# Optimization experiments

Hardware: AMD Instinct MI355X
Metric: run time of the kernel (lower is better)

## Reference

```python
import jax, jax.numpy as jnp
import numpy as np

B, S, E, H, WIN = 16, 4096, 512, 8, 64


def setup_inputs() -> dict:
    key = jax.random.key(0)
    k1, k2, k3 = jax.random.split(key, 3)
    bound = 1.0 / np.sqrt(E)
    x = jax.random.normal(k1, (B, S, E), dtype=jnp.float32)
    # nn.MultiheadAttention params: packed in-projection (3E, E) + bias, out-projection (E, E) + bias
    W_in = jax.random.uniform(k2, (3 * E, E), minval=-bound, maxval=bound, dtype=jnp.float32)
    b_in = jnp.zeros((3 * E,), dtype=jnp.float32)
    W_out = jax.random.uniform(k3, (E, E), minval=-bound, maxval=bound, dtype=jnp.float32)
    b_out = jnp.zeros((E,), dtype=jnp.float32)
    return {"x": x, "W_in": W_in, "b_in": b_in, "W_out": W_out, "b_out": b_out}


def reference(x, W_in, b_in, W_out, b_out):
    # Faithful to the torch module: nn.MultiheadAttention has batch_first=False,
    # over the batch axis, with window positions acting as the MHA batch.
    Bb, Ss, Ee = x.shape
    Dh = Ee // H
    nW = Ss // WIN
    xp = x.reshape(Bb, nW, WIN, Ee).transpose(1, 2, 0, 3)
    qkv = xp @ W_in.T + b_in
    q, k, v = jnp.split(qkv, 3, axis=-1)
    q = q.reshape(nW, WIN, Bb, H, Dh)
    k = k.reshape(nW, WIN, Bb, H, Dh)
    v = v.reshape(nW, WIN, Bb, H, Dh)
    scale = 1.0 / np.sqrt(Dh)
    scores = jnp.einsum('nwahd,nwbhd->nwhab', q, k) * scale
    attn = jax.nn.softmax(scores, axis=-1)
    o = jnp.einsum('nwhab,nwbhd->nwahd', attn, v).reshape(nW, WIN, Bb, Ee)
    out = o @ W_out.T + b_out
    return out.transpose(2, 0, 1, 3).reshape(Bb, Ss, Ee)
```

## Files before the change

kernel.cpp:

```cpp
#include <hip/hip_runtime.h>


#define S_LEN  4096
#define E_DIM  512
#define QKV_LD 1536

typedef __bf16 bf16x8 __attribute__((ext_vector_type(8)));
typedef __bf16 bf16x4 __attribute__((ext_vector_type(4)));
typedef short  s16x4  __attribute__((ext_vector_type(4)));
typedef float  f32x4  __attribute__((ext_vector_type(4)));

__device__ __forceinline__ float b2f(unsigned int u16) {
    return __uint_as_float(u16 << 16);
}
__device__ __forceinline__ unsigned short f2bf(float f) {
    unsigned int u = __float_as_uint(f);
    u += 0x7fffu + ((u >> 16) & 1u);
    return (unsigned short)(u >> 16);
}
__device__ __forceinline__ void unpack8(uint4 u, float* f) {
    f[0] = b2f(u.x & 0xffffu); f[1] = b2f(u.x >> 16);
    f[2] = b2f(u.y & 0xffffu); f[3] = b2f(u.y >> 16);
    f[4] = b2f(u.z & 0xffffu); f[5] = b2f(u.z >> 16);
    f[6] = b2f(u.w & 0xffffu); f[7] = b2f(u.w >> 16);
}
__device__ __forceinline__ uint4 pack8(const float* f) {
    uint4 u;
    u.x = (unsigned)f2bf(f[0]) | ((unsigned)f2bf(f[1]) << 16);
    u.y = (unsigned)f2bf(f[2]) | ((unsigned)f2bf(f[3]) << 16);
    u.z = (unsigned)f2bf(f[4]) | ((unsigned)f2bf(f[5]) << 16);
    u.w = (unsigned)f2bf(f[6]) | ((unsigned)f2bf(f[7]) << 16);
    return u;
}

__device__ __forceinline__ bool detect_f32(const unsigned int* __restrict__ probe) {
    unsigned int w = probe[threadIdx.x & 63];
    unsigned int e = (w >> 23) & 0xffu;
    unsigned long long b = __ballot(e >= 90u && e <= 160u);
    return __popcll(b) >= 32;
}

__device__ __forceinline__ void gload16(const unsigned short* g, unsigned short* l) {
    __builtin_amdgcn_global_load_lds(
        (const __attribute__((address_space(1))) unsigned int*)g,
        (__attribute__((address_space(3))) unsigned int*)l, 16, 0, 0);
}

__device__ __forceinline__ f32x4 mfma16bf(s16x4 a, s16x4 b, f32x4 c) {
    f32x4 d;
    asm volatile("s_nop 3\n\t"
                 "v_mfma_f32_16x16x16_bf16 %0, %1, %2, %3\n\t"
                 "s_nop 7\n\t"
                 "s_nop 7"
                 : "=v"(d) : "v"(a), "v"(b), "v"(c));
    return d;
}

template<bool F32>
__device__ __forceinline__ uint4 cvt8(const void* src, long off) {
    if (F32) {
        const float* p = (const float*)src + off;
        float4 a = *(const float4*)p, b = *(const float4*)(p + 4);
        float f[8] = {a.x, a.y, a.z, a.w, b.x, b.y, b.z, b.w};
        return pack8(f);
    }
    return *(const uint4*)((const unsigned short*)src + off);
}

template<bool F32>
__device__ void conv_w_body(const void* Win, const void* Wout, const void* bin,
                            const void* bout, unsigned short* dst)
{
    int c = blockIdx.x * 256 + threadIdx.x;
    if (c >= 131328) return;
    const void* src; long soff; long doff = (long)c * 8;
    if (c < 98304)       { src = Win;  soff = doff; }
    else if (c < 131072) { src = Wout; soff = doff - 786432; }
    else if (c < 131264) { src = bin;  soff = doff - 1048576; }
    else                 { src = bout; soff = doff - 1050112; }
    *(uint4*)(dst + doff) = cvt8<F32>(src, soff);
}
__global__ __launch_bounds__(256) void conv_w_k(const void* Win, const void* Wout,
        const void* bin, const void* bout, unsigned short* dst,
        const unsigned int* __restrict__ probe)
{
    if (detect_f32(probe)) conv_w_body<true>(Win, Wout, bin, bout, dst);
    else                   conv_w_body<false>(Win, Wout, bin, bout, dst);
}

template<bool F32>
__device__ void conv_x_body(const void* __restrict__ x, unsigned short* __restrict__ xb,
                            int s0, int lgC)
{
    long c = (long)blockIdx.x * 256 + threadIdx.x;
    const long row = c >> 6;
    const int  col = (int)(c & 63) * 8;
    const long srcRow = (row >> lgC) * S_LEN + s0 + (row & ((1L << lgC) - 1));
    *(uint4*)(xb + row * E_DIM + col) = cvt8<F32>(x, srcRow * E_DIM + col);
}
__global__ __launch_bounds__(256) void conv_x_k(const void* __restrict__ x,
        unsigned short* __restrict__ xb, int s0, int lgC,
        const unsigned int* __restrict__ probe)
{
    if (detect_f32(probe)) conv_x_body<true>(x, xb, s0, lgC);
    else                   conv_x_body<false>(x, xb, s0, lgC);
}

template<int BM, int BN, int WM, int WN, int MODE>
__device__ void gemm8_body(const unsigned short* __restrict__ A,
                           const unsigned short* __restrict__ W,
                           const unsigned short* __restrict__ bias,
                           void* __restrict__ C, int s0, int lgC, int nbx,
                           bool f32out)
{
    constexpr int MF   = BM / WM / 16;
    constexpr int NF   = BN / WN / 16;
    constexpr int NL   = (BM + BN) / 64;
    constexpr int TILE = (BM + BN) * 64;
    constexpr int NT   = E_DIM / 64;
    constexpr int lda  = (MODE == 1) ? E_DIM : QKV_LD;

    __shared__ __align__(16) unsigned short Ls[2 * TILE];

    const int nwg = gridDim.x;
    const int id0 = blockIdx.x;
    const int id  = (id0 & 7) * (nwg >> 3) + (id0 >> 3);
    const int bx  = id % nbx;
    const int by  = id / nbx;

    const int tid  = threadIdx.x;
    const int wave = tid >> 6;
    const int lane = tid & 63;
    const int wm   = wave / WN;
    const int wn   = wave % WN;
    const int lrow = lane & 15;
    const int lq   = lane >> 4;
    const long m0  = (long)bx * BM;
    const int  n0  = by * BN;

    const unsigned short* src[NL];
    unsigned short*       dst[NL];
    #pragma unroll
    for (int j = 0; j < NL; ++j) {
        const int Lg  = wave * NL + j;
        const int row = Lg * 8 + (lane >> 3);
        const int ls  = (lane & 7) ^ (row & 7);
        src[j] = (row < BM) ? A + (m0 + row) * lda + ls * 8
                            : W + (long)(n0 + row - BM) * E_DIM + ls * 8;
        dst[j] = Ls + Lg * 512;
    }

    f32x4 acc[MF][NF];
    #pragma unroll
    for (int i = 0; i < MF; ++i)
        #pragma unroll
        for (int j = 0; j < NF; ++j)
            acc[i][j] = (f32x4){0.f, 0.f, 0.f, 0.f};

    #pragma unroll
    for (int j = 0; j < NL; ++j) gload16(src[j], dst[j]);

    int buf = 0;
    #pragma unroll
    for (int it = 0; it < NT; ++it) {
        __builtin_amdgcn_s_barrier();
        asm volatile("" ::: "memory");
        if (it + 1 < NT) {
            #pragma unroll
            for (int j = 0; j < NL; ++j)
                gload16(src[j] + (it + 1) * 64, dst[j] + (buf ^ 1) * TILE);
            asm volatile("s_waitcnt vmcnt(%0)" :: "n"(NL) : "memory");
        } else {
            asm volatile("s_waitcnt vmcnt(0)" ::: "memory");
        }
        __builtin_amdgcn_sched_barrier(0);
        __builtin_amdgcn_s_barrier();
        asm volatile("" ::: "memory");

        const unsigned short* Ab = Ls + buf * TILE;
        const unsigned short* Bb = Ab + BM * 64;
        #pragma unroll
        for (int ks = 0; ks < 2; ++ks) {
            bf16x8 bfr[NF];
            #pragma unroll
            for (int ni = 0; ni < NF; ++ni) {
                const int r = wn * (BN / WN) + ni * 16 + lrow;
                bfr[ni] = *(const bf16x8*)(Bb + r * 64 + (((ks * 4 + lq) ^ (r & 7)) << 3));
            }
            #pragma unroll
            for (int mh = 0; mh < MF; mh += 4) {
                bf16x8 afr[4];
                #pragma unroll
                for (int u = 0; u < 4; ++u) {
                    const int r = wm * (BM / WM) + (mh + u) * 16 + lrow;
                    afr[u] = *(const bf16x8*)(Ab + r * 64 + (((ks * 4 + lq) ^ (r & 7)) << 3));
                }
                __builtin_amdgcn_s_setprio(1);
                #pragma unroll
                for (int u = 0; u < 4; ++u)
                    #pragma unroll
                    for (int ni = 0; ni < NF; ++ni)
                        acc[mh + u][ni] = __builtin_amdgcn_mfma_f32_16x16x32_bf16(
                            afr[u], bfr[ni], acc[mh + u][ni], 0, 0, 0);
                __builtin_amdgcn_s_setprio(0);
            }
        }
        __builtin_amdgcn_sched_barrier(0);
        buf ^= 1;
    }

    #pragma unroll
    for (int mi = 0; mi < MF; ++mi)
        #pragma unroll
        for (int ni = 0; ni < NF; ++ni) {
            const int col = n0 + wn * (BN / WN) + ni * 16 + lrow;
            const float bv = b2f(bias[col]);
            #pragma unroll
            for (int r = 0; r < 4; ++r) {
                const long row = m0 + wm * (BM / WM) + mi * 16 + lq * 4 + r;
                const float v = acc[mi][ni][r] + bv;
                if (MODE == 1) {
                    ((unsigned short*)C)[row * QKV_LD + col] = f2bf(v);
                } else {
                    const long g = ((row >> lgC) * S_LEN + s0 + (row & ((1L << lgC) - 1)))
                                   * E_DIM + col;
                    if (f32out) ((float*)C)[g] = v;
                    else        ((unsigned short*)C)[g] = f2bf(v);
                }
            }
        }
}

__global__ __launch_bounds__(512, 2) void gemm1_k(const unsigned short* __restrict__ A,
        const unsigned short* __restrict__ W, const unsigned short* __restrict__ bias,
        unsigned short* __restrict__ C, int nbx)
{
    gemm8_body<256, 256, 2, 4, 1>(A, W, bias, C, 0, 0, nbx, false);
}

__global__ __launch_bounds__(512, 2) void gemm2_k(const unsigned short* __restrict__ A,
        const unsigned short* __restrict__ W, const unsigned short* __restrict__ bias,
        void* __restrict__ C, int s0, int lgC, int nbx,
        const unsigned int* __restrict__ probe)
{
    const bool f32out = detect_f32(probe);
    gemm8_body<256, 128, 4, 2, 2>(A, W, bias, C, s0, lgC, nbx, f32out);
}

__global__ __launch_bounds__(256) void attn_kernel(unsigned short* __restrict__ qkv,
                                                   int Cs)
{
    const int wave = threadIdx.x >> 6;
    const int lane = threadIdx.x & 63;
    const int task = blockIdx.x * 4 + wave;
    const int h    = task & 7;
    const int sc   = task >> 3;
    const int a    = lane & 15;
    const int g    = lane >> 4;

    const unsigned short* qbase =
        qkv + ((long)a * Cs + sc) * QKV_LD + h * 64 + g * 8;
    const bf16x8 qf0 = *(const bf16x8*)(qbase);
    const bf16x8 qf1 = *(const bf16x8*)(qbase + 32);
    const bf16x8 kf0 = *(const bf16x8*)(qbase + 512);
    const bf16x8 kf1 = *(const bf16x8*)(qbase + 544);

    unsigned short vv[4][4];
    const unsigned short* vbase = qkv + (long)sc * QKV_LD + 1024 + h * 64 + a;
    #pragma unroll
    for (int j = 0; j < 4; ++j) {
        const unsigned short* vr = vbase + (long)(g * 4 + j) * Cs * QKV_LD;
        #pragma unroll
        for (int t = 0; t < 4; ++t) vv[t][j] = vr[t * 16];
    }

    f32x4 s = (f32x4){0.f, 0.f, 0.f, 0.f};
    s = __builtin_amdgcn_mfma_f32_16x16x32_bf16(kf0, qf0, s, 0, 0, 0);
    s = __builtin_amdgcn_mfma_f32_16x16x32_bf16(kf1, qf1, s, 0, 0, 0);

    float m = fmaxf(fmaxf(s[0], s[1]), fmaxf(s[2], s[3]));
    m = fmaxf(m, __shfl_xor(m, 16));
    m = fmaxf(m, __shfl_xor(m, 32));
    float p[4], sum = 0.f;
    #pragma unroll
    for (int r = 0; r < 4; ++r) { p[r] = __expf((s[r] - m) * 0.125f); sum += p[r]; }
    sum += __shfl_xor(sum, 16);
    sum += __shfl_xor(sum, 32);
    const float inv = 1.f / sum;

    bf16x4 phi, plo;
    #pragma unroll
    for (int r = 0; r < 4; ++r) {
        const float pn = p[r] * inv;
        const __bf16 hi = (__bf16)pn;
        phi[r] = hi;
        plo[r] = (__bf16)(pn - (float)hi);
    }
    const s16x4 phs = __builtin_bit_cast(s16x4, phi);
    const s16x4 pls = __builtin_bit_cast(s16x4, plo);

    unsigned short* obase = qkv + ((long)a * Cs + sc) * QKV_LD + h * 64 + g * 4;
    const f32x4 zero = (f32x4){0.f, 0.f, 0.f, 0.f};
    #pragma unroll
    for (int t = 0; t < 4; ++t) {
        s16x4 vf;
        #pragma unroll
        for (int j = 0; j < 4; ++j) vf[j] = (short)vv[t][j];
        f32x4 o = mfma16bf(vf, phs, zero);
        o = mfma16bf(vf, pls, o);
        uint2 st;
        st.x = (unsigned)f2bf(o[0]) | ((unsigned)f2bf(o[1]) << 16);
        st.y = (unsigned)f2bf(o[2]) | ((unsigned)f2bf(o[3]) << 16);
        *(uint2*)(obase + t * 16) = st;
    }
}

extern "C" void kernel_launch(void* const* d_in, const int* in_sizes, int n_in,
                              void* d_out, int out_size, void* d_ws, size_t ws_size,
                              hipStream_t stream)
{
    const void* x     = d_in[0];
    const void* W_in  = d_in[1];
    const void* b_in  = d_in[2];
    const void* W_out = d_in[3];
    const void* b_out = d_in[4];
    const unsigned int* probe = (const unsigned int*)d_in[0];

    const bool big = ws_size >= 270536704ull;
    const int  Cs  = big ? S_LEN : 1024;
    const int  lgC = big ? 12 : 10;
    const int  nch = big ? 1 : 4;
    const long M   = 16L * Cs;
    const int  nbx = (int)(M / 256);

    unsigned short* qkv = (unsigned short*)d_ws;
    unsigned short* xb  = qkv + (size_t)M * QKV_LD;
    unsigned short* wb  = xb + (size_t)M * E_DIM;
    const unsigned short* Wi = wb;
    const unsigned short* Wo = wb + 786432;
    const unsigned short* bi = wb + 1048576;
    const unsigned short* bo = wb + 1050112;

    hipLaunchKernelGGL(conv_w_k, dim3(514), dim3(256), 0, stream,
                       W_in, W_out, b_in, b_out, wb, probe);

    for (int c = 0; c < nch; ++c) {
        const int s0 = c * Cs;
        hipLaunchKernelGGL(conv_x_k, dim3((int)(M / 4)), dim3(256), 0, stream,
                           x, xb, s0, lgC, probe);
        hipLaunchKernelGGL(gemm1_k, dim3(nbx * 6), dim3(512), 0, stream,
                           xb, Wi, bi, qkv, nbx);
        hipLaunchKernelGGL(attn_kernel, dim3(Cs * 2), dim3(256), 0, stream, qkv, Cs);
        hipLaunchKernelGGL(gemm2_k, dim3(nbx * 4), dim3(512), 0, stream,
                           qkv, Wo, bo, d_out, s0, lgC, nbx, probe);
    }
}
```

Before: 481.5 us.

## Deepen GEMM pipeline to 4-stage ring with BK=32 and swap tile traversal order

The GEMM mainloop now uses a K-step of 32 with a 4-slot LDS ring buffer, keeping three tiles of global-to-LDS loads in flight instead of double buffering with BK=64. The swizzle and LDS read addressing are adjusted for 32-wide rows, and the tail waits are graded. Block-index mapping is also changed so consecutive workgroups walk along N before M, which changes L2 reuse of A versus W tiles. The goal is better hiding of memory latency. The cost is twice as many barriers per K and LDS usage that stays the same or grows.

```diff
diff --git a/kernel.cpp b/kernel.cpp
--- a/kernel.cpp
+++ b/kernel.cpp
@@ -44,6 +44,11 @@
     __builtin_amdgcn_global_load_lds(
         (const __attribute__((address_space(1))) unsigned int*)g,
         (__attribute__((address_space(3))) unsigned int*)l, 16, 0, 0);
+}
+
+template<int N>
+__device__ __forceinline__ void waitvm() {
+    asm volatile("s_waitcnt vmcnt(%0)" :: "n"(N) : "memory");
 }
 
 __device__ __forceinline__ f32x4 mfma16bf(s16x4 a, s16x4 b, f32x4 c) {
@@ -113,20 +118,23 @@
                            void* __restrict__ C, int s0, int lgC, int nbx,
                            bool f32out)
 {
+    constexpr int BK   = 32;
     constexpr int MF   = BM / WM / 16;
     constexpr int NF   = BN / WN / 16;
-    constexpr int NL   = (BM + BN) / 64;
-    constexpr int TILE = (BM + BN) * 64;
-    constexpr int NT   = E_DIM / 64;
+    constexpr int NL   = (BM + BN) * BK / 256 / 16;
+    constexpr int TILE = (BM + BN) * BK;
+    constexpr int NT   = E_DIM / BK;
+    constexpr int PF   = 3;
     constexpr int lda  = (MODE == 1) ? E_DIM : QKV_LD;
 
-    __shared__ __align__(16) unsigned short Ls[2 * TILE];
+    __shared__ __align__(16) unsigned short Ls[4 * TILE];
 
     const int nwg = gridDim.x;
     const int id0 = blockIdx.x;
     const int id  = (id0 & 7) * (nwg >> 3) + (id0 >> 3);
-    const int bx  = id % nbx;
-    const int by  = id / nbx;
+    const int nby = nwg / nbx;
+    const int by  = id % nby;
+    const int bx  = id / nby;
 
     const int tid  = threadIdx.x;
     const int wave = tid >> 6;
@@ -143,8 +151,8 @@
     #pragma unroll
     for (int j = 0; j < NL; ++j) {
         const int Lg  = wave * NL + j;
-        const int row = Lg * 8 + (lane >> 3);
-        const int ls  = (lane & 7) ^ (row & 7);
+        const int row = Lg * 16 + (lane >> 2);
+        const int ls  = (lane & 3) ^ ((row >> 1) & 3);
         src[j] = (row < BM) ? A + (m0 + row) * lda + ls * 8
                             : W + (long)(n0 + row - BM) * E_DIM + ls * 8;
         dst[j] = Ls + Lg * 512;
@@ -158,55 +166,57 @@
             acc[i][j] = (f32x4){0.f, 0.f, 0.f, 0.f};
 
     #pragma unroll
-    for (int j = 0; j < NL; ++j) gload16(src[j], dst[j]);
-
-    int buf = 0;
+    for (int t = 0; t < PF; ++t)
+        #pragma unroll
+        for (int j = 0; j < NL; ++j)
+            gload16(src[j] + t * BK, dst[j] + t * TILE);
+
     #pragma unroll
     for (int it = 0; it < NT; ++it) {
         __builtin_amdgcn_s_barrier();
         asm volatile("" ::: "memory");
-        if (it + 1 < NT) {
+        if (it + PF < NT) {
             #pragma unroll
             for (int j = 0; j < NL; ++j)
-                gload16(src[j] + (it + 1) * 64, dst[j] + (buf ^ 1) * TILE);
-            asm volatile("s_waitcnt vmcnt(%0)" :: "n"(NL) : "memory");
+                gload16(src[j] + (it + PF) * BK, dst[j] + ((it + PF) & 3) * TILE);
+            waitvm<PF * NL>();
+        } else if (NT - 1 - it == 2) {
+            waitvm<2 * NL>();
+        } else if (NT - 1 - it == 1) {
+            waitvm<NL>();
         } else {
-            asm volatile("s_waitcnt vmcnt(0)" ::: "memory");
+            waitvm<0>();
         }
         __builtin_amdgcn_sched_barrier(0);
         __builtin_amdgcn_s_barrier();
         asm volatile("" ::: "memory");
 
-        const unsigned short* Ab = Ls + buf * TILE;
-        const unsigned short* Bb = Ab + BM * 64;
-        #pragma unroll
-        for (int ks = 0; ks < 2; ++ks) {
-            bf16x8 bfr[NF];
+        const unsigned short* Ab = Ls + (it & 3) * TILE;
+        const unsigned short* Bb = Ab + BM * BK;
+        bf16x8 bfr[NF];
+        #pragma unroll
+        for (int ni = 0; ni < NF; ++ni) {
+            const int r = wn * (BN / WN) + ni * 16 + lrow;
+            bfr[ni] = *(const bf16x8*)(Bb + r * 32 + ((lq ^ ((r >> 1) & 3)) << 3));
+        }
+        #pragma unroll
+        for (int mh = 0; mh < MF; mh += 4) {
+            bf16x8 afr[4];
             #pragma unroll
-            for (int ni = 0; ni < NF; ++ni) {
-                const int r = wn * (BN / WN) + ni * 16 + lrow;
-                bfr[ni] = *(const bf16x8*)(Bb + r * 64 + (((ks * 4 + lq) ^ (r & 7)) << 3));
+            for (int u = 0; u < 4; ++u) {
+                const int r = wm * (BM / WM) + (mh + u) * 16 + lrow;
+                afr[u] = *(const bf16x8*)(Ab + r * 32 + ((lq ^ ((r >> 1) & 3)) << 3));
             }
+            __builtin_amdgcn_s_setprio(1);
             #pragma unroll
-            for (int mh = 0; mh < MF; mh += 4) {
-                bf16x8 afr[4];
+            for (int u = 0; u < 4; ++u)
                 #pragma unroll
-                for (int u = 0; u < 4; ++u) {
-                    const int r = wm * (BM / WM) + (mh + u) * 16 + lrow;
-                    afr[u] = *(const bf16x8*)(Ab + r * 64 + (((ks * 4 + lq) ^ (r & 7)) << 3));
-                }
-                __builtin_amdgcn_s_setprio(1);
-                #pragma unroll
-                for (int u = 0; u < 4; ++u)
-                    #pragma unroll
-                    for (int ni = 0; ni < NF; ++ni)
-                        acc[mh + u][ni] = __builtin_amdgcn_mfma_f32_16x16x32_bf16(
-                            afr[u], bfr[ni], acc[mh + u][ni], 0, 0, 0);
-                __builtin_amdgcn_s_setprio(0);
-            }
+                for (int ni = 0; ni < NF; ++ni)
+                    acc[mh + u][ni] = __builtin_amdgcn_mfma_f32_16x16x32_bf16(
+                        afr[u], bfr[ni], acc[mh + u][ni], 0, 0, 0);
+            __builtin_amdgcn_s_setprio(0);
         }
         __builtin_amdgcn_sched_barrier(0);
-        buf ^= 1;
     }
 
     #pragma unroll
```

Result: no change. 480.5 us (-0.2%).
